# Performance work log

Measured on AMD Instinct MI355X. Metric: run time of the kernel, lower is better.

Reference implementation:

```python
import jax, jax.numpy as jnp
import numpy as np


def setup_inputs() -> dict:
    key = jax.random.key(0)
    ks = jax.random.split(key, 7)
    N, D, K = 500000, 128, 32
    return {
        "x": jax.random.normal(ks[0], (N, D), dtype=jnp.float32),
        "h_e": jax.random.normal(ks[1], (N, D), dtype=jnp.float32),
        "bond_n": jax.random.uniform(ks[2], (K, N), dtype=jnp.float32),
        "W_i_w": jax.random.normal(ks[3], (D, 2 * D), dtype=jnp.float32) * 0.05,
        "W_i_b": jax.random.normal(ks[4], (D,), dtype=jnp.float32) * 0.05,
        "W_m_w": jax.random.normal(ks[5], (D, D), dtype=jnp.float32) * 0.05,
        "W_m_b": jax.random.normal(ks[6], (D,), dtype=jnp.float32) * 0.05,
    }


def reference(x, h_e, bond_n, W_i_w, W_i_b, W_m_w, W_m_b):
    # h_n = relu(W_i([x ; h_e]))  -> [N, D]
    h_n = jax.nn.relu(jnp.concatenate([x, h_e], axis=1) @ W_i_w.T + W_i_b)
    # m = sum_k sum_n bond_n[k,n] * h_n[n,:]  -> [D]
    # (equivalent to torch: (bond_n[...,None] * h_n).sum(1).sum(0),
    #  but expressed as a contraction to avoid the [K,N,D] intermediate)
    m = jnp.einsum('kn,nd->d', bond_n, h_n)
    # h = relu(h_n + W_m(m))  -> [N, D] via broadcast of the [D] message
    h = jax.nn.relu(h_n + (m @ W_m_w.T + W_m_b))
    return h
```

## Files before the change

kernel.cpp:

```cpp
#include <hip/hip_runtime.h>
#include <stdint.h>
#include <stddef.h>

#define N_ROWS 500000
#define DDIM   128
#define K2     256
#define KBOND  32
#define TILE_ROWS 64
#define NT ((N_ROWS + TILE_ROWS - 1) / TILE_ROWS)
#define MR_CH 64
#define NCH ((NT + MR_CH - 1) / MR_CH)
#define P2_BLOCKS 2048

typedef float  f32x4  __attribute__((ext_vector_type(4)));
typedef __bf16 bf16x8 __attribute__((ext_vector_type(8)));
typedef __bf16 bf16x4 __attribute__((ext_vector_type(4)));

__device__ __bf16 g_wbf[DDIM * K2];
__device__ float  g_partials[(size_t)NT * DDIM];
__device__ float  g_p2[NCH * DDIM];
__device__ float  g_msg[DDIM];
__device__ __bf16 g_hn[(size_t)N_ROWS * DDIM];

__global__ void k_prep(const float* __restrict__ w) {
  int t = blockIdx.x * blockDim.x + threadIdx.x;
  if (t < DDIM * K2) g_wbf[t] = (__bf16)w[t];
}

__global__ __launch_bounds__(512)
void k_pass1(const float* __restrict__ x, const float* __restrict__ he,
             const float* __restrict__ bond, const float* __restrict__ bias)
{
  __shared__ __align__(16) unsigned char a_lds[TILE_ROWS * 512];
  __shared__ float s_part[8][TILE_ROWS];
  __shared__ float s_lds[TILE_ROWS];

  const int tid  = threadIdx.x;
  const int w    = tid >> 6;
  const int lane = tid & 63;
  const int l15  = lane & 15;
  const int g    = lane >> 4;
  const int rb   = blockIdx.x * TILE_ROWS;

  bf16x8 wfrag[8];
  #pragma unroll
  for (int ks = 0; ks < 8; ++ks)
    wfrag[ks] = *(const bf16x8*)(g_wbf + (size_t)(16 * w + l15) * K2 + ks * 32 + 8 * g);

  const int d0 = 16 * w + 4 * g;
  const f32x4 bv = *(const f32x4*)(bias + d0);

  #pragma unroll
  for (int it = 0; it < 4; ++it) {
    const int r = ((it & 1) ? 32 : 0) + (tid >> 4);
    const int c = tid & 15;
    const float* src = (it < 2) ? x : he;
    int n  = rb + r;
    int nc = n < N_ROWS ? n : (N_ROWS - 1);
    f32x4 v0 = *(const f32x4*)(src + (size_t)nc * DDIM + 8 * c);
    f32x4 v1 = *(const f32x4*)(src + (size_t)nc * DDIM + 8 * c + 4);
    bf16x8 b;
    #pragma unroll
    for (int i = 0; i < 4; ++i) { b[i] = (__bf16)v0[i]; b[4 + i] = (__bf16)v1[i]; }
    const int base = (it < 2) ? 0 : 256;
    *(bf16x8*)(a_lds + r * 512 + ((base + 16 * c) ^ ((r & 15) << 4))) = b;
  }

  {
    const int row = tid & 63, kg = tid >> 6;
    int n = rb + row;
    float p = 0.f;
    if (n < N_ROWS) {
      #pragma unroll
      for (int j = 0; j < 4; ++j) p += bond[(size_t)(4 * kg + j) * N_ROWS + n];
    }
    s_part[kg][row] = p;
  }
  __syncthreads();

  if (tid < TILE_ROWS) {
    float s = 0.f;
    #pragma unroll
    for (int kg = 0; kg < 8; ++kg) s += s_part[kg][tid];
    s_lds[tid] = s;
  }

  f32x4 acc[4];
  #pragma unroll
  for (int i = 0; i < 4; ++i) acc[i] = (f32x4)(0.f);

  #pragma unroll
  for (int ks = 0; ks < 8; ++ks) {
    bf16x8 bfrag[4];
    #pragma unroll
    for (int nf = 0; nf < 4; ++nf) {
      const int r = 16 * nf + l15;
      bfrag[nf] = *(const bf16x8*)(a_lds + r * 512 +
                                   ((64 * ks + 16 * g) ^ ((r & 15) << 4)));
    }
    #pragma unroll
    for (int nf = 0; nf < 4; ++nf)
      acc[nf] = __builtin_amdgcn_mfma_f32_16x16x32_bf16(wfrag[ks], bfrag[nf],
                                                        acc[nf], 0, 0, 0);
  }
  __syncthreads();

  f32x4 macc = (f32x4)(0.f);
  #pragma unroll
  for (int nf = 0; nf < 4; ++nf) {
    const int lr = 16 * nf + l15;
    const int n  = rb + lr;
    const float sn = s_lds[lr];
    f32x4 h;
    #pragma unroll
    for (int i = 0; i < 4; ++i) {
      float v = acc[nf][i] + bv[i];
      h[i] = v > 0.f ? v : 0.f;
    }
    macc += sn * h;
    if (n < N_ROWS) {
      bf16x4 hb;
      #pragma unroll
      for (int i = 0; i < 4; ++i) hb[i] = (__bf16)h[i];
      *(bf16x4*)(g_hn + (size_t)n * DDIM + d0) = hb;
    }
  }

  #pragma unroll
  for (int off = 1; off <= 8; off <<= 1) {
    #pragma unroll
    for (int i = 0; i < 4; ++i) macc[i] += __shfl_xor(macc[i], off, 64);
  }
  if (l15 == 0)
    *(f32x4*)(&g_partials[(size_t)blockIdx.x * DDIM + d0]) = macc;
}

__global__ void k_mr1() {
  const int c  = blockIdx.x;
  const int r0 = c * MR_CH;
  const int d    = threadIdx.x & 127;
  const int half = threadIdx.x >> 7;
  const int rend = (r0 + MR_CH < NT) ? (r0 + MR_CH) : NT;
  float acc = 0.f;
  for (int r = r0 + half; r < rend; r += 2)
    acc += g_partials[(size_t)r * DDIM + d];
  __shared__ float sp[DDIM];
  if (half == 0) sp[d] = acc;
  __syncthreads();
  if (half == 1) g_p2[c * DDIM + d] = sp[d] + acc;
}

__global__ void k_msg(const float* __restrict__ wm, const float* __restrict__ bm) {
  __shared__ float ms[DDIM];
  const int d = threadIdx.x;
  float s = 0.f;
  for (int c = 0; c < NCH; ++c) s += g_p2[c * DDIM + d];
  ms[d] = s;
  __syncthreads();
  float acc = bm[d];
  #pragma unroll 8
  for (int j = 0; j < DDIM; ++j) acc += ms[j] * wm[(size_t)d * DDIM + j];
  g_msg[d] = acc;
}

__global__ __launch_bounds__(256)
void k_pass2(float* __restrict__ out)
{
  __shared__ float ms[DDIM];
  if (threadIdx.x < DDIM) ms[threadIdx.x] = g_msg[threadIdx.x];
  __syncthreads();
  const size_t total = (size_t)N_ROWS * DDIM / 8;
  for (size_t c = (size_t)blockIdx.x * blockDim.x + threadIdx.x; c < total;
       c += (size_t)gridDim.x * blockDim.x) {
    const size_t base = c * 8;
    const int col0 = (int)(base & (DDIM - 1));
    bf16x8 hv = *(const bf16x8*)(g_hn + base);
    f32x4 o0, o1;
    #pragma unroll
    for (int i = 0; i < 4; ++i) {
      float a = (float)hv[i]     + ms[col0 + i];
      float b = (float)hv[4 + i] + ms[col0 + 4 + i];
      o0[i] = a > 0.f ? a : 0.f;
      o1[i] = b > 0.f ? b : 0.f;
    }
    *(f32x4*)(out + base)     = o0;
    *(f32x4*)(out + base + 4) = o1;
  }
}

extern "C" void kernel_launch(void* const* d_in, const int* in_sizes, int n_in,
                              void* d_out, int out_size, void* d_ws, size_t ws_size,
                              hipStream_t stream) {
  const float* x    = (const float*)d_in[0];
  const float* he   = (const float*)d_in[1];
  const float* bond = (const float*)d_in[2];
  const float* wi   = (const float*)d_in[3];
  const float* bi   = (const float*)d_in[4];
  const float* wm   = (const float*)d_in[5];
  const float* bm   = (const float*)d_in[6];
  float* out = (float*)d_out;
  (void)d_ws; (void)ws_size;

  k_prep<<<(DDIM * K2 + 255) / 256, 256, 0, stream>>>(wi);
  k_pass1<<<NT, 512, 0, stream>>>(x, he, bond, bi);
  k_mr1<<<NCH, 256, 0, stream>>>();
  k_msg<<<1, 128, 0, stream>>>(wm, bm);
  k_pass2<<<P2_BLOCKS, 256, 0, stream>>>(out);
}
```

Measured before the change: 284.8 us.

## Make pass1 persistent with double-buffered async LDS loads and separate bond reduction

Pass1 becomes a persistent kernel of 512 blocks that walks 32-row tiles. While the MFMA work runs on the current tile, it prefetches the next tile's raw fp32 x/h_e rows into a second LDS buffer using global_load_lds, and converts to bf16 when reading fragments. The bond row-sum moves into its own k_s kernel that writes g_s. The per-block partials shrink to 512, so the intermediate reduction kernel is dropped and merged into k_msg. The goal is to hide global load latency and reduce launch and reduction overhead, at the cost of an extra pass over bond, doubled LDS footprint in fp32, and reliance on N divisible by 32.

```diff
diff --git a/kernel.cpp b/kernel.cpp
--- a/kernel.cpp
+++ b/kernel.cpp
@@ -6,10 +6,9 @@
 #define DDIM   128
 #define K2     256
 #define KBOND  32
-#define TILE_ROWS 64
-#define NT ((N_ROWS + TILE_ROWS - 1) / TILE_ROWS)
-#define MR_CH 64
-#define NCH ((NT + MR_CH - 1) / MR_CH)
+#define TILE2  32
+#define NT2    (N_ROWS / TILE2)
+#define NB     512
 #define P2_BLOCKS 2048
 
 typedef float  f32x4  __attribute__((ext_vector_type(4)));
@@ -17,8 +16,8 @@
 typedef __bf16 bf16x4 __attribute__((ext_vector_type(4)));
 
 __device__ __bf16 g_wbf[DDIM * K2];
-__device__ float  g_partials[(size_t)NT * DDIM];
-__device__ float  g_p2[NCH * DDIM];
+__device__ float  g_s[N_ROWS];
+__device__ float  g_partials[NB * DDIM];
 __device__ float  g_msg[DDIM];
 __device__ __bf16 g_hn[(size_t)N_ROWS * DDIM];
 
@@ -27,103 +26,117 @@
   if (t < DDIM * K2) g_wbf[t] = (__bf16)w[t];
 }
 
-__global__ __launch_bounds__(512)
+__global__ __launch_bounds__(256)
+void k_s(const float* __restrict__ bond) {
+  int n = blockIdx.x * 256 + threadIdx.x;
+  if (n >= N_ROWS) return;
+  float a = 0.f, b = 0.f;
+  #pragma unroll
+  for (int k = 0; k < KBOND; k += 2) {
+    a += bond[(size_t)k * N_ROWS + n];
+    b += bond[(size_t)(k + 1) * N_ROWS + n];
+  }
+  g_s[n] = a + b;
+}
+
+static __device__ __forceinline__ void gload16(const float* g, float* l) {
+  __builtin_amdgcn_global_load_lds(
+      (const __attribute__((address_space(1))) void*)g,
+      (__attribute__((address_space(3))) void*)l, 16, 0, 0);
+}
+
+__global__ __launch_bounds__(512, 4)
 void k_pass1(const float* __restrict__ x, const float* __restrict__ he,
-             const float* __restrict__ bond, const float* __restrict__ bias)
+             const float* __restrict__ bias)
 {
-  __shared__ __align__(16) unsigned char a_lds[TILE_ROWS * 512];
-  __shared__ float s_part[8][TILE_ROWS];
-  __shared__ float s_lds[TILE_ROWS];
+  __shared__ float a_lds[2][TILE2 * K2];
 
   const int tid  = threadIdx.x;
   const int w    = tid >> 6;
   const int lane = tid & 63;
   const int l15  = lane & 15;
   const int g    = lane >> 4;
-  const int rb   = blockIdx.x * TILE_ROWS;
 
   bf16x8 wfrag[8];
   #pragma unroll
   for (int ks = 0; ks < 8; ++ks)
-    wfrag[ks] = *(const bf16x8*)(g_wbf + (size_t)(16 * w + l15) * K2 + ks * 32 + 8 * g);
+    wfrag[ks] = *(const bf16x8*)(g_wbf + (size_t)(16 * w + l15) * K2 + 32 * ks + 8 * g);
 
   const int d0 = 16 * w + 4 * g;
   const f32x4 bv = *(const f32x4*)(bias + d0);
 
-  #pragma unroll
-  for (int it = 0; it < 4; ++it) {
-    const int r = ((it & 1) ? 32 : 0) + (tid >> 4);
-    const int c = tid & 15;
-    const float* src = (it < 2) ? x : he;
-    int n  = rb + r;
-    int nc = n < N_ROWS ? n : (N_ROWS - 1);
-    f32x4 v0 = *(const f32x4*)(src + (size_t)nc * DDIM + 8 * c);
-    f32x4 v1 = *(const f32x4*)(src + (size_t)nc * DDIM + 8 * c + 4);
-    bf16x8 b;
-    #pragma unroll
-    for (int i = 0; i < 4; ++i) { b[i] = (__bf16)v0[i]; b[4 + i] = (__bf16)v1[i]; }
-    const int base = (it < 2) ? 0 : 256;
-    *(bf16x8*)(a_lds + r * 512 + ((base + 16 * c) ^ ((r & 15) << 4))) = b;
-  }
-
+  const float* sbase = ((lane < 32) ? x : he) + 4 * ((lane & 31) ^ w);
+
+  f32x4 macc = (f32x4)(0.f);
+
+  int t = blockIdx.x;
   {
-    const int row = tid & 63, kg = tid >> 6;
-    int n = rb + row;
-    float p = 0.f;
-    if (n < N_ROWS) {
-      #pragma unroll
-      for (int j = 0; j < 4; ++j) p += bond[(size_t)(4 * kg + j) * N_ROWS + n];
-    }
-    s_part[kg][row] = p;
-  }
-  __syncthreads();
-
-  if (tid < TILE_ROWS) {
-    float s = 0.f;
-    #pragma unroll
-    for (int kg = 0; kg < 8; ++kg) s += s_part[kg][tid];
-    s_lds[tid] = s;
-  }
-
-  f32x4 acc[4];
-  #pragma unroll
-  for (int i = 0; i < 4; ++i) acc[i] = (f32x4)(0.f);
-
-  #pragma unroll
-  for (int ks = 0; ks < 8; ++ks) {
-    bf16x8 bfrag[4];
-    #pragma unroll
-    for (int nf = 0; nf < 4; ++nf) {
-      const int r = 16 * nf + l15;
-      bfrag[nf] = *(const bf16x8*)(a_lds + r * 512 +
-                                   ((64 * ks + 16 * g) ^ ((r & 15) << 4)));
-    }
-    #pragma unroll
-    for (int nf = 0; nf < 4; ++nf)
-      acc[nf] = __builtin_amdgcn_mfma_f32_16x16x32_bf16(wfrag[ks], bfrag[nf],
-                                                        acc[nf], 0, 0, 0);
-  }
-  __syncthreads();
-
-  f32x4 macc = (f32x4)(0.f);
-  #pragma unroll
-  for (int nf = 0; nf < 4; ++nf) {
-    const int lr = 16 * nf + l15;
-    const int n  = rb + lr;
-    const float sn = s_lds[lr];
-    f32x4 h;
-    #pragma unroll
-    for (int i = 0; i < 4; ++i) {
-      float v = acc[nf][i] + bv[i];
-      h[i] = v > 0.f ? v : 0.f;
-    }
-    macc += sn * h;
-    if (n < N_ROWS) {
-      bf16x4 hb;
-      #pragma unroll
-      for (int i = 0; i < 4; ++i) hb[i] = (__bf16)h[i];
-      *(bf16x4*)(g_hn + (size_t)n * DDIM + d0) = hb;
-    }
+    const size_t rowb = (size_t)(t * TILE2 + w) * DDIM;
+    #pragma unroll
+    for (int j = 0; j < 4; ++j)
+      gload16(sbase + rowb + (size_t)(8 * j) * DDIM,
+              &a_lds[0][(512 * j + 64 * w) * 4]);
+  }
+  float s0 = g_s[t * TILE2 + l15];
+  float s1 = g_s[t * TILE2 + 16 + l15];
+  __syncthreads();
+
+  int cur = 0;
+  while (true) {
+    const int  tn  = t + NB;
+    const bool has = tn < NT2;
+    float s0n = 0.f, s1n = 0.f;
+
+    if (has) {
+      const size_t rowb = (size_t)(tn * TILE2 + w) * DDIM;
+      #pragma unroll
+      for (int j = 0; j < 4; ++j)
+        gload16(sbase + rowb + (size_t)(8 * j) * DDIM,
+                &a_lds[cur ^ 1][(512 * j + 64 * w) * 4]);
+      s0n = g_s[tn * TILE2 + l15];
+      s1n = g_s[tn * TILE2 + 16 + l15];
+    }
+
+    f32x4 acc0 = (f32x4)(0.f), acc1 = (f32x4)(0.f);
+    const char* base = (const char*)&a_lds[cur][0];
+    const int sw = (l15 & 7) << 4;
+    #pragma unroll
+    for (int ks = 0; ks < 8; ++ks) {
+      const int o = 128 * ks + 32 * g;
+      f32x4 u0 = *(const f32x4*)(base + l15 * 1024        + ((o)      ^ sw));
+      f32x4 u1 = *(const f32x4*)(base + l15 * 1024        + ((o + 16) ^ sw));
+      f32x4 v0 = *(const f32x4*)(base + (16 + l15) * 1024 + ((o)      ^ sw));
+      f32x4 v1 = *(const f32x4*)(base + (16 + l15) * 1024 + ((o + 16) ^ sw));
+      bf16x8 b0, b1;
+      #pragma unroll
+      for (int i = 0; i < 4; ++i) {
+        b0[i] = (__bf16)u0[i]; b0[4 + i] = (__bf16)u1[i];
+        b1[i] = (__bf16)v0[i]; b1[4 + i] = (__bf16)v1[i];
+      }
+      acc0 = __builtin_amdgcn_mfma_f32_16x16x32_bf16(wfrag[ks], b0, acc0, 0, 0, 0);
+      acc1 = __builtin_amdgcn_mfma_f32_16x16x32_bf16(wfrag[ks], b1, acc1, 0, 0, 0);
+    }
+
+    __syncthreads();
+
+    {
+      const int rb = t * TILE2;
+      f32x4 h0, h1;
+      #pragma unroll
+      for (int i = 0; i < 4; ++i) {
+        float a = acc0[i] + bv[i]; h0[i] = a > 0.f ? a : 0.f;
+        float b = acc1[i] + bv[i]; h1[i] = b > 0.f ? b : 0.f;
+      }
+      macc += s0 * h0 + s1 * h1;
+      bf16x4 hb0, hb1;
+      #pragma unroll
+      for (int i = 0; i < 4; ++i) { hb0[i] = (__bf16)h0[i]; hb1[i] = (__bf16)h1[i]; }
+      *(bf16x4*)(g_hn + (size_t)(rb + l15) * DDIM + d0)      = hb0;
+      *(bf16x4*)(g_hn + (size_t)(rb + 16 + l15) * DDIM + d0) = hb1;
+    }
+
+    if (!has) break;
+    cur ^= 1; t = tn; s0 = s0n; s1 = s1n;
   }
 
   #pragma unroll
@@ -135,32 +148,23 @@
     *(f32x4*)(&g_partials[(size_t)blockIdx.x * DDIM + d0]) = macc;
 }
 
-__global__ void k_mr1() {
-  const int c  = blockIdx.x;
-  const int r0 = c * MR_CH;
+__global__ void k_msg(const float* __restrict__ wm, const float* __restrict__ bm) {
+  __shared__ float ms[DDIM];
+  __shared__ float sp[DDIM];
   const int d    = threadIdx.x & 127;
   const int half = threadIdx.x >> 7;
-  const int rend = (r0 + MR_CH < NT) ? (r0 + MR_CH) : NT;
-  float acc = 0.f;
-  for (int r = r0 + half; r < rend; r += 2)
-    acc += g_partials[(size_t)r * DDIM + d];
-  __shared__ float sp[DDIM];
-  if (half == 0) sp[d] = acc;
-  __syncthreads();
-  if (half == 1) g_p2[c * DDIM + d] = sp[d] + acc;
-}
-
-__global__ void k_msg(const float* __restrict__ wm, const float* __restrict__ bm) {
-  __shared__ float ms[DDIM];
-  const int d = threadIdx.x;
   float s = 0.f;
-  for (int c = 0; c < NCH; ++c) s += g_p2[c * DDIM + d];
-  ms[d] = s;
-  __syncthreads();
-  float acc = bm[d];
-  #pragma unroll 8
-  for (int j = 0; j < DDIM; ++j) acc += ms[j] * wm[(size_t)d * DDIM + j];
-  g_msg[d] = acc;
+  for (int c = half; c < NB; c += 2) s += g_partials[c * DDIM + d];
+  if (half == 0) sp[d] = s;
+  __syncthreads();
+  if (half == 1) ms[d] = sp[d] + s;
+  __syncthreads();
+  if (half == 0) {
+    float acc = bm[d];
+    #pragma unroll 8
+    for (int j = 0; j < DDIM; ++j) acc += ms[j] * wm[(size_t)d * DDIM + j];
+    g_msg[d] = acc;
+  }
 }
 
 __global__ __launch_bounds__(256)
@@ -202,8 +206,8 @@
   (void)d_ws; (void)ws_size;
 
   k_prep<<<(DDIM * K2 + 255) / 256, 256, 0, stream>>>(wi);
-  k_pass1<<<NT, 512, 0, stream>>>(x, he, bond, bi);
-  k_mr1<<<NCH, 256, 0, stream>>>();
-  k_msg<<<1, 128, 0, stream>>>(wm, bm);
+  k_s<<<(N_ROWS + 255) / 256, 256, 0, stream>>>(bond);
+  k_pass1<<<NB, 512, 0, stream>>>(x, he, bi);
+  k_msg<<<1, 256, 0, stream>>>(wm, bm);
   k_pass2<<<P2_BLOCKS, 256, 0, stream>>>(out);
 }
```

New measurement: 315.8 us. 1.11x slower.
